# Optimization experiments

Hardware: AMD Instinct MI355X
Metric: run time of the kernel (lower is better)

Reference implementation:

```python
import jax, jax.numpy as jnp
import numpy as np

B, SEQ, D = 2, 1024, 768
E, H = 8, 3072          # num_experts, expert hidden (mlp_ratio=4)
CAPACITY = 2            # k = CAPACITY * num_tokens


def setup_inputs() -> dict:
    key = jax.random.key(0)
    ks = jax.random.split(key, 6)
    x = jax.random.normal(ks[0], (B, SEQ, D), dtype=jnp.float32)
    gate_weight = jax.random.normal(ks[1], (E, D), dtype=jnp.float32) * 0.006
    w1 = jax.random.normal(ks[2], (E, D, H), dtype=jnp.float32) * (1.0 / np.sqrt(D))
    b1 = jnp.zeros((E, H), dtype=jnp.float32)
    w2 = jax.random.normal(ks[3], (E, H, D), dtype=jnp.float32) * (1.0 / np.sqrt(H))
    b2 = jnp.zeros((E, D), dtype=jnp.float32)
    return {"x": x, "gate_weight": gate_weight, "w1": w1, "b1": b1, "w2": w2, "b2": b2}


def reference(x, gate_weight, w1, b1, w2, b2):
    Bb, s, d = x.shape
    xf = x.reshape(-1, d)                     # [S, D]
    S = xf.shape[0]
    k = S * CAPACITY
    logits = xf @ gate_weight.T               # [S, E]
    scores = jax.nn.softmax(logits, axis=-1).T  # [E, S]
    # flattened top-k over all (expert, token) pairs -> sparse gate matrix
    vals, idx = jax.lax.top_k(scores.reshape(-1), k)
    gate = jnp.zeros((E * S,), dtype=x.dtype).at[idx].add(vals).reshape(E, S)
    # expert MLPs (GELU-tanh) applied per expert; zero gate entries kill
    # non-routed (expert, token) pairs -> same math as gather/MLP/scatter.
    h = jax.nn.gelu(jnp.einsum('sd,edh->esh', xf, w1) + b1[:, None, :], approximate=True)
    out = jnp.einsum('esh,ehd->esd', h, w2) + b2[:, None, :]   # [E, S, D]
    y = jnp.einsum('es,esd->sd', gate, out)    # weighted combine + sum over experts
    return y.reshape(Bb, s, d)
```

## Files before the change

kernel.cpp:

```cpp
#include <hip/hip_runtime.h>
#include <math.h>

#define S_TOK 2048
#define NEXP  8
#define DDIM  768
#define HDIM  3072
#define KSEL  4096

typedef __attribute__((ext_vector_type(8))) short short8;
typedef __attribute__((ext_vector_type(4))) float f32x4;
typedef __attribute__((ext_vector_type(2))) unsigned int u32x2;

#define GLOAD_LDS(GP, LP)                                            \
  __builtin_amdgcn_global_load_lds(                                  \
      (__attribute__((address_space(1))) void*)(GP),                 \
      (__attribute__((address_space(3))) void*)(LP), 16, 0, 0)

__device__ __forceinline__ unsigned short f2bf(float f) {
  unsigned u = __float_as_uint(f);
  u += 0x7fffu + ((u >> 16) & 1u);
  return (unsigned short)(u >> 16);
}

__device__ __forceinline__ float gelu_fast(float v) {
  float u = 0.7978845608028654f * (v + 0.044715f * v * v * v);
  float t = __expf(-2.0f * fabsf(u));
  float th = (1.0f - t) / (1.0f + t);
  th = copysignf(th, u);
  return 0.5f * v * (1.0f + th);
}

__global__ __launch_bounds__(256) void zero_kernel(float* __restrict__ p, int n) {
  int i = blockIdx.x * 256 + threadIdx.x;
  if (i < n) p[i] = 0.f;
}

__global__ __launch_bounds__(256) void convx_kernel(const float* __restrict__ x,
                                                    short* __restrict__ xb) {
  int i = (blockIdx.x * 256 + threadIdx.x) * 8;
  float4 a = *(const float4*)(x + i);
  float4 b = *(const float4*)(x + i + 4);
  short8 v;
  v[0] = (short)f2bf(a.x); v[1] = (short)f2bf(a.y);
  v[2] = (short)f2bf(a.z); v[3] = (short)f2bf(a.w);
  v[4] = (short)f2bf(b.x); v[5] = (short)f2bf(b.y);
  v[6] = (short)f2bf(b.z); v[7] = (short)f2bf(b.w);
  *(short8*)(xb + i) = v;
}

__global__ __launch_bounds__(256) void convw_kernel(
    const float* __restrict__ src, short* __restrict__ dst,
    int ncols_src, int col0, int ncols_dst, int row0, int nrows, int nrows_src)
{
  long long i = ((long long)blockIdx.x * 256 + threadIdx.x) * 8;
  int n = (int)(i % ncols_dst);
  long long rr = i / ncols_dst;
  int r = (int)(rr % nrows);
  int e = (int)(rr / nrows);
  const float* s = src + ((size_t)e * nrows_src + row0 + r) * ncols_src + col0 + n;
  float4 a = *(const float4*)(s);
  float4 b = *(const float4*)(s + 4);
  short8 v;
  v[0] = (short)f2bf(a.x); v[1] = (short)f2bf(a.y);
  v[2] = (short)f2bf(a.z); v[3] = (short)f2bf(a.w);
  v[4] = (short)f2bf(b.x); v[5] = (short)f2bf(b.y);
  v[6] = (short)f2bf(b.z); v[7] = (short)f2bf(b.w);
  *(short8*)(dst + i) = v;
}

__global__ __launch_bounds__(256) void gate_kernel(
    const float* __restrict__ x, const float* __restrict__ gw,
    float* __restrict__ scores)
{
  int tid  = threadIdx.x;
  int lane = tid & 63;
  int wid  = tid >> 6;
  int token = blockIdx.x * 4 + wid;
  const float* xr = x + (size_t)token * DDIM;

  float acc[NEXP];
#pragma unroll
  for (int e = 0; e < NEXP; ++e) acc[e] = 0.f;

  for (int d = lane; d < DDIM; d += 64) {
    float xv = xr[d];
#pragma unroll
    for (int e = 0; e < NEXP; ++e) acc[e] += xv * gw[e * DDIM + d];
  }
#pragma unroll
  for (int e = 0; e < NEXP; ++e) {
    for (int off = 32; off; off >>= 1) acc[e] += __shfl_down(acc[e], off, 64);
  }
  if (lane == 0) {
    float m = acc[0];
#pragma unroll
    for (int e = 1; e < NEXP; ++e) m = fmaxf(m, acc[e]);
    float p[NEXP], s = 0.f;
#pragma unroll
    for (int e = 0; e < NEXP; ++e) { p[e] = expf(acc[e] - m); s += p[e]; }
    float inv = 1.0f / s;
#pragma unroll
    for (int e = 0; e < NEXP; ++e) scores[e * S_TOK + token] = p[e] * inv;
  }
}

__device__ unsigned block_scan_excl(unsigned v, volatile unsigned* wsum) {
  int tid = threadIdx.x, lane = tid & 63, wid = tid >> 6;
  __syncthreads();
  unsigned x = v;
#pragma unroll
  for (int off = 1; off < 64; off <<= 1) {
    unsigned t = __shfl_up(x, off, 64);
    if (lane >= off) x += t;
  }
  if (lane == 63) wsum[wid] = x;
  __syncthreads();
  if (tid < 64) {
    unsigned w = (lane < 16) ? wsum[lane] : 0u;
#pragma unroll
    for (int off = 1; off < 16; off <<= 1) {
      unsigned t = __shfl_up(w, off, 64);
      if (lane >= off) w += t;
    }
    if (lane < 16) wsum[lane] = w;
  }
  __syncthreads();
  unsigned woff = (wid > 0) ? wsum[wid - 1] : 0u;
  return woff + (x - v);
}

__global__ __launch_bounds__(1024) void select_kernel(
    const float* __restrict__ scores,
    int* __restrict__ tokenlist, float* __restrict__ slotgate,
    int* __restrict__ offsets)
{
  __shared__ unsigned cnt;
  __shared__ unsigned wsum[16];
  int tid = threadIdx.x;
  int base = tid * 16;

  float sv[16]; unsigned key[16];
#pragma unroll
  for (int j = 0; j < 16; ++j) {
    sv[j] = scores[base + j];
    key[j] = __float_as_uint(sv[j]);
  }

  unsigned lo = 0, hi = 0x3F800000u;
  while (lo < hi) {
    unsigned mid = lo + ((hi - lo + 1) >> 1);
    if (tid == 0) cnt = 0;
    __syncthreads();
    unsigned c = 0;
#pragma unroll
    for (int j = 0; j < 16; ++j) c += (key[j] >= mid) ? 1u : 0u;
    for (int off = 32; off; off >>= 1) c += __shfl_down(c, off, 64);
    if ((tid & 63) == 0) atomicAdd(&cnt, c);
    __syncthreads();
    unsigned tot = cnt;
    __syncthreads();
    if (tot >= (unsigned)KSEL) lo = mid; else hi = mid - 1;
  }
  unsigned V = lo;

  if (tid == 0) cnt = 0;
  __syncthreads();
  {
    unsigned c = 0;
#pragma unroll
    for (int j = 0; j < 16; ++j) c += (key[j] > V) ? 1u : 0u;
    for (int off = 32; off; off >>= 1) c += __shfl_down(c, off, 64);
    if ((tid & 63) == 0) atomicAdd(&cnt, c);
  }
  __syncthreads();
  int need = KSEL - (int)cnt;
  __syncthreads();

  unsigned tloc = 0;
#pragma unroll
  for (int j = 0; j < 16; ++j) tloc += (key[j] == V) ? 1u : 0u;
  unsigned texcl = block_scan_excl(tloc, wsum);

  unsigned selmask = 0, sloc = 0, trun = texcl;
#pragma unroll
  for (int j = 0; j < 16; ++j) {
    bool f;
    if (key[j] > V) f = true;
    else if (key[j] == V) { f = ((int)trun < need); ++trun; }
    else f = false;
    if (f) { selmask |= (1u << j); ++sloc; }
  }
  unsigned sexcl = block_scan_excl(sloc, wsum);

  if ((tid & 127) == 0) offsets[tid >> 7] = (int)sexcl;
  if (tid == 0) offsets[NEXP] = KSEL;

  unsigned p = sexcl;
#pragma unroll
  for (int j = 0; j < 16; ++j) {
    int i = base + j;
    if (selmask & (1u << j)) {
      tokenlist[p] = i & (S_TOK - 1);
      slotgate[p] = sv[j];
      ++p;
    }
  }
}

template <int MODE>
__global__ __launch_bounds__(256) void moe_mfma(
    const short* __restrict__ Abase, const short* __restrict__ Wbf,
    const float* __restrict__ bias, void* __restrict__ outp,
    const int* __restrict__ offsets, const int* __restrict__ tokenlist,
    const float* __restrict__ slotgate,
    int N, int SA, int estride, int split_bits, int cbias, int bias_en)
{
  const int e = (int)blockIdx.x;
  const int tile  = (int)blockIdx.z >> split_bits;
  const int split = (int)blockIdx.z & ((1 << split_bits) - 1);
  const int kb = split * 768;

  const int r0 = offsets[e];
  const int rows = offsets[e + 1] - r0;
  const int rowbase = tile << 7;
  if (rowbase >= rows) return;
  int vr = rows - rowbase; if (vr > 128) vr = 128;
  const int colbase = (int)blockIdx.y << 7;

  __shared__ __align__(16) short As[128 * 32];
  __shared__ __align__(16) short Bs[64 * 64];
  const unsigned bs_lds = (unsigned)(uintptr_t)&Bs[0];

  const int tid = threadIdx.x;
  const int lane = tid & 63;
  const int wid = tid >> 6;
  const int wr = (wid >> 1) << 6;
  const int wc = (wid & 1) << 6;
  const int l15 = lane & 15;
  const int lq = lane >> 4;

  const int row0 = (wid * 2) * 16 + (lane >> 2);
  const int row1 = row0 + 16;
  const int cr0 = (row0 < vr) ? row0 : (vr - 1);
  const int cr1 = (row1 < vr) ? row1 : (vr - 1);
  const short *aptr0, *aptr1;
  if (MODE == 1) {
    aptr0 = Abase + (size_t)tokenlist[r0 + rowbase + cr0] * SA + ((lane & 3) << 3);
    aptr1 = Abase + (size_t)tokenlist[r0 + rowbase + cr1] * SA + ((lane & 3) << 3);
  } else {
    aptr0 = Abase + (size_t)(r0 + rowbase + cr0) * SA + kb + ((lane & 3) << 3);
    aptr1 = Abase + (size_t)(r0 + rowbase + cr1) * SA + kb + ((lane & 3) << 3);
  }

  const short* wb = Wbf + (size_t)e * estride + colbase +
                    ((lane >> 3) << 4) + ((lane & 1) << 3) +
                    (size_t)(kb + ((lane & 7) >> 1)) * N;
  const short* bptr0 = wb + (size_t)(wid * 2 + 0) * 4 * N;
  const short* bptr1 = wb + (size_t)(wid * 2 + 1) * 4 * N;

  const int dst0 = wid * 1024;
  const int dst1 = wid * 1024 + 512;

#define STAGE(K0)                                                 \
  {                                                               \
    GLOAD_LDS(aptr0 + (K0), As + dst0);                           \
    GLOAD_LDS(aptr1 + (K0), As + dst1);                           \
    GLOAD_LDS(bptr0 + (size_t)(K0) * N, Bs + dst0);               \
    GLOAD_LDS(bptr1 + (size_t)(K0) * N, Bs + dst1);               \
  }

  f32x4 acc[4][4];
#pragma unroll
  for (int i = 0; i < 4; ++i)
#pragma unroll
    for (int j = 0; j < 4; ++j) acc[i][j] = (f32x4){0.f, 0.f, 0.f, 0.f};

  STAGE(0);

#pragma unroll 1
  for (int k0 = 0; k0 < 768; k0 += 32) {
    __syncthreads();
    short8 af[4], bfr[4];
#pragma unroll
    for (int i = 0; i < 4; ++i)
      af[i] = *(const short8*)&As[(wr + i * 16 + l15) * 32 + lq * 8];
#pragma unroll
    for (int j = 0; j < 4; ++j) {
      unsigned off = bs_lds + ((unsigned)((lq << 4) + (wc >> 4) + j) << 7) +
                     ((unsigned)l15 << 3);
      union { short8 s; u32x2 u[2]; } fb;
      asm volatile("ds_read_b64_tr_b16 %0, %2 offset:0\n\t"
                   "ds_read_b64_tr_b16 %1, %2 offset:1024"
                   : "=&v"(fb.u[0]), "=&v"(fb.u[1]) : "v"(off));
      bfr[j] = fb.s;
    }
    asm volatile("s_waitcnt lgkmcnt(0)" ::: "memory");
    __builtin_amdgcn_sched_barrier(0);
    __syncthreads();
    if (k0 + 32 < 768) STAGE(k0 + 32);
#pragma unroll
    for (int i = 0; i < 4; ++i)
#pragma unroll
      for (int j = 0; j < 4; ++j)
        acc[i][j] = __builtin_amdgcn_mfma_f32_16x16x32_bf16(af[i], bfr[j], acc[i][j], 0, 0, 0);
  }

  if (MODE == 1) {
    short* hb = (short*)outp;
    const float* bp = bias + (size_t)e * HDIM + cbias + colbase;
#pragma unroll
    for (int i = 0; i < 4; ++i) {
      int rb = wr + i * 16 + lq * 4;
#pragma unroll
      for (int j = 0; j < 4; ++j) {
        int col = wc + j * 16 + l15;
        float bvv = bp[col];
#pragma unroll
        for (int p = 0; p < 4; ++p) {
          int r = rb + p;
          if (r < vr)
            hb[(size_t)(r0 + rowbase + r) * N + colbase + col] =
                (short)f2bf(gelu_fast(acc[i][j][p] + bvv));
        }
      }
    }
  } else {
    float* y = (float*)outp;
    const float* bp = bias + (size_t)e * DDIM + colbase;
    const int addb = (bias_en && split == 0);
#pragma unroll
    for (int i = 0; i < 4; ++i) {
      int rb = wr + i * 16 + lq * 4;
#pragma unroll
      for (int p = 0; p < 4; ++p) {
        int r = rb + p;
        if (r < vr) {
          int gi = r0 + rowbase + r;
          float g = slotgate[gi];
          float* yrow = y + (size_t)tokenlist[gi] * DDIM + colbase;
#pragma unroll
          for (int j = 0; j < 4; ++j) {
            int col = wc + j * 16 + l15;
            float v = acc[i][j][p] + (addb ? bp[col] : 0.f);
            atomicAdd(&yrow[col], g * v);
          }
        }
      }
    }
  }
#undef STAGE
}

extern "C" void kernel_launch(void* const* d_in, const int* in_sizes, int n_in,
                              void* d_out, int out_size, void* d_ws, size_t ws_size,
                              hipStream_t stream) {
  const float* x  = (const float*)d_in[0];
  const float* gw = (const float*)d_in[1];
  const float* w1 = (const float*)d_in[2];
  const float* b1 = (const float*)d_in[3];
  const float* w2 = (const float*)d_in[4];
  const float* b2 = (const float*)d_in[5];
  float* y = (float*)d_out;

  char* ws = (char*)d_ws;
  float* scores    = (float*)(ws);
  int*   tokenlist = (int*)(ws + (64 << 10));
  float* slotgate  = (float*)(ws + (80 << 10));
  int*   offsets   = (int*)(ws + (96 << 10));
  short* xbf       = (short*)(ws + (128 << 10));

  const size_t head = (size_t)(128 << 10) + (size_t)S_TOK * DDIM * 2;
  int nchunk = 2;
  {
    size_t need1 = head + (size_t)NEXP * DDIM * HDIM * 2 + (size_t)KSEL * HDIM * 2;
    if (ws_size >= need1) nchunk = 1;
  }
  const int NC = HDIM / nchunk;
  short* wbf  = (short*)(ws + head);
  short* hbuf = wbf + (size_t)NEXP * DDIM * NC;
  const int estride = DDIM * NC;
  const int sb2 = (NC == 3072) ? 2 : 1;

  zero_kernel<<<(out_size + 255) / 256, 256, 0, stream>>>(y, out_size);
  convx_kernel<<<S_TOK * DDIM / 2048, 256, 0, stream>>>(x, xbf);
  gate_kernel<<<S_TOK / 4, 256, 0, stream>>>(x, gw, scores);
  select_kernel<<<1, 1024, 0, stream>>>(scores, tokenlist, slotgate, offsets);

  for (int c = 0; c < nchunk; ++c) {
    convw_kernel<<<(NEXP * DDIM * NC) / 2048, 256, 0, stream>>>(
        w1, wbf, HDIM, c * NC, NC, 0, DDIM, DDIM);
    dim3 g1(NEXP, NC / 128, 16);
    moe_mfma<1><<<g1, 256, 0, stream>>>(xbf, wbf, b1, hbuf, offsets, tokenlist,
                                        slotgate, NC, DDIM, estride, 0, c * NC, 1);
    convw_kernel<<<(NEXP * NC * DDIM) / 2048, 256, 0, stream>>>(
        w2, wbf, DDIM, 0, DDIM, c * NC, NC, HDIM);
    dim3 g2(NEXP, DDIM / 128, 16 << sb2);
    moe_mfma<2><<<g2, 256, 0, stream>>>(hbuf, wbf, b2, y, offsets, tokenlist,
                                        slotgate, DDIM, NC, estride, sb2, 0, c == 0);
  }
}
```

Baseline: 230.6 us.

## Double-buffer LDS tiles in grouped expert GEMM with explicit vmcnt waits

Splits the A and B shared-memory tiles into two ping-pong buffers and issues global-to-LDS loads two k-steps ahead. Each k-step waits only for the older batch of loads via a partial vmcnt wait before the barrier, so loads overlap with the MFMA work of the previous step. The cost is double the LDS per block, which can lower occupancy, plus hand-managed waitcnt logic that has to stay in step with how many loads are in flight.

```diff
diff --git a/kernel.cpp b/kernel.cpp
--- a/kernel.cpp
+++ b/kernel.cpp
@@ -227,9 +227,12 @@
   int vr = rows - rowbase; if (vr > 128) vr = 128;
   const int colbase = (int)blockIdx.y << 7;
 
-  __shared__ __align__(16) short As[128 * 32];
-  __shared__ __align__(16) short Bs[64 * 64];
-  const unsigned bs_lds = (unsigned)(uintptr_t)&Bs[0];
+  __shared__ __align__(16) short As0[128 * 32];
+  __shared__ __align__(16) short As1[128 * 32];
+  __shared__ __align__(16) short Bs0[64 * 64];
+  __shared__ __align__(16) short Bs1[64 * 64];
+  const unsigned bs0_lds = (unsigned)(uintptr_t)&Bs0[0];
+  const unsigned bs1_lds = (unsigned)(uintptr_t)&Bs1[0];
 
   const int tid = threadIdx.x;
   const int lane = tid & 63;
@@ -261,12 +264,12 @@
   const int dst0 = wid * 1024;
   const int dst1 = wid * 1024 + 512;
 
-#define STAGE(K0)                                                 \
+#define STAGE(K0, ASX, BSX)                                       \
   {                                                               \
-    GLOAD_LDS(aptr0 + (K0), As + dst0);                           \
-    GLOAD_LDS(aptr1 + (K0), As + dst1);                           \
-    GLOAD_LDS(bptr0 + (size_t)(K0) * N, Bs + dst0);               \
-    GLOAD_LDS(bptr1 + (size_t)(K0) * N, Bs + dst1);               \
+    GLOAD_LDS(aptr0 + (K0), (ASX) + dst0);                        \
+    GLOAD_LDS(aptr1 + (K0), (ASX) + dst1);                        \
+    GLOAD_LDS(bptr0 + (size_t)(K0) * N, (BSX) + dst0);            \
+    GLOAD_LDS(bptr1 + (size_t)(K0) * N, (BSX) + dst1);            \
   }
 
   f32x4 acc[4][4];
@@ -275,34 +278,45 @@
 #pragma unroll
     for (int j = 0; j < 4; ++j) acc[i][j] = (f32x4){0.f, 0.f, 0.f, 0.f};
 
-  STAGE(0);
+#define KSTEP_BODY(ASX, BLDS, STG_COND, STG_K, STG_AS, STG_BS, LASTWAIT)   \
+  {                                                               \
+    if (LASTWAIT) { asm volatile("s_waitcnt vmcnt(0)" ::: "memory"); }     \
+    else          { asm volatile("s_waitcnt vmcnt(4)" ::: "memory"); }     \
+    __builtin_amdgcn_s_barrier();                                 \
+    __builtin_amdgcn_sched_barrier(0);                            \
+    short8 af[4], bfr[4];                                         \
+    _Pragma("unroll")                                             \
+    for (int i = 0; i < 4; ++i)                                   \
+      af[i] = *(const short8*)&ASX[(wr + i * 16 + l15) * 32 + lq * 8];     \
+    _Pragma("unroll")                                             \
+    for (int j = 0; j < 4; ++j) {                                 \
+      unsigned off = (BLDS) + ((unsigned)((lq << 4) + (wc >> 4) + j) << 7) + \
+                     ((unsigned)l15 << 3);                        \
+      union { short8 s; u32x2 u[2]; } fb;                         \
+      asm volatile("ds_read_b64_tr_b16 %0, %2 offset:0\n\t"       \
+                   "ds_read_b64_tr_b16 %1, %2 offset:1024"        \
+                   : "=&v"(fb.u[0]), "=&v"(fb.u[1]) : "v"(off));  \
+      bfr[j] = fb.s;                                              \
+    }                                                             \
+    asm volatile("s_waitcnt lgkmcnt(0)" ::: "memory");            \
+    __builtin_amdgcn_sched_barrier(0);                            \
+    __builtin_amdgcn_s_barrier();                                 \
+    __builtin_amdgcn_sched_barrier(0);                            \
+    if (STG_COND) STAGE(STG_K, STG_AS, STG_BS);                   \
+    _Pragma("unroll")                                             \
+    for (int i = 0; i < 4; ++i)                                   \
+      _Pragma("unroll")                                           \
+      for (int j = 0; j < 4; ++j)                                 \
+        acc[i][j] = __builtin_amdgcn_mfma_f32_16x16x32_bf16(af[i], bfr[j], acc[i][j], 0, 0, 0); \
+  }
+
+  STAGE(0, As0, Bs0);
+  STAGE(32, As1, Bs1);
 
 #pragma unroll 1
-  for (int k0 = 0; k0 < 768; k0 += 32) {
-    __syncthreads();
-    short8 af[4], bfr[4];
-#pragma unroll
-    for (int i = 0; i < 4; ++i)
-      af[i] = *(const short8*)&As[(wr + i * 16 + l15) * 32 + lq * 8];
-#pragma unroll
-    for (int j = 0; j < 4; ++j) {
-      unsigned off = bs_lds + ((unsigned)((lq << 4) + (wc >> 4) + j) << 7) +
-                     ((unsigned)l15 << 3);
-      union { short8 s; u32x2 u[2]; } fb;
-      asm volatile("ds_read_b64_tr_b16 %0, %2 offset:0\n\t"
-                   "ds_read_b64_tr_b16 %1, %2 offset:1024"
-                   : "=&v"(fb.u[0]), "=&v"(fb.u[1]) : "v"(off));
-      bfr[j] = fb.s;
-    }
-    asm volatile("s_waitcnt lgkmcnt(0)" ::: "memory");
-    __builtin_amdgcn_sched_barrier(0);
-    __syncthreads();
-    if (k0 + 32 < 768) STAGE(k0 + 32);
-#pragma unroll
-    for (int i = 0; i < 4; ++i)
-#pragma unroll
-      for (int j = 0; j < 4; ++j)
-        acc[i][j] = __builtin_amdgcn_mfma_f32_16x16x32_bf16(af[i], bfr[j], acc[i][j], 0, 0, 0);
+  for (int k0 = 0; k0 < 768; k0 += 64) {
+    KSTEP_BODY(As0, bs0_lds, (k0 + 64 < 768), k0 + 64, As0, Bs0, false);
+    KSTEP_BODY(As1, bs1_lds, (k0 + 96 < 768), k0 + 96, As1, Bs1, (k0 >= 704));
   }
 
   if (MODE == 1) {
@@ -349,6 +363,7 @@
     }
   }
 #undef STAGE
+#undef KSTEP_BODY
 }
 
 extern "C" void kernel_launch(void* const* d_in, const int* in_sizes, int n_in,
```

New measurement: 219.7 us. -4.7%, faster.

## Transpose weights during bf16 conversion, double-buffer GEMM LDS, fuse x conversion into gate

Applied to the files above, without the earlier changes.

The weight-conversion kernel now writes bf16 weights transposed (N-major, K contiguous) through a 32x32 LDS tile, so the GEMM can load B the same way as A and read it with plain 16-byte LDS reads instead of transpose reads. The GEMM main loop becomes double-buffered: the next K-slab is issued before computing the current one, leaving one barrier per iteration. The bf16 conversion of x is folded into the gate kernel, which removes one launch. The trade-off is a transpose kernel that makes scalar 2-byte stores and uses a strided LDS pattern, so it may convert weights more slowly than the old vectorized 8-wide converter. Doubling LDS to 32 KB per block may also lower occupancy.

```diff
diff --git a/kernel.cpp b/kernel.cpp
--- a/kernel.cpp
+++ b/kernel.cpp
@@ -9,7 +9,6 @@
 
 typedef __attribute__((ext_vector_type(8))) short short8;
 typedef __attribute__((ext_vector_type(4))) float f32x4;
-typedef __attribute__((ext_vector_type(2))) unsigned int u32x2;
 
 #define GLOAD_LDS(GP, LP)                                            \
   __builtin_amdgcn_global_load_lds(                                  \
@@ -35,48 +34,39 @@
   if (i < n) p[i] = 0.f;
 }
 
-__global__ __launch_bounds__(256) void convx_kernel(const float* __restrict__ x,
-                                                    short* __restrict__ xb) {
-  int i = (blockIdx.x * 256 + threadIdx.x) * 8;
-  float4 a = *(const float4*)(x + i);
-  float4 b = *(const float4*)(x + i + 4);
-  short8 v;
-  v[0] = (short)f2bf(a.x); v[1] = (short)f2bf(a.y);
-  v[2] = (short)f2bf(a.z); v[3] = (short)f2bf(a.w);
-  v[4] = (short)f2bf(b.x); v[5] = (short)f2bf(b.y);
-  v[6] = (short)f2bf(b.z); v[7] = (short)f2bf(b.w);
-  *(short8*)(xb + i) = v;
-}
-
-__global__ __launch_bounds__(256) void convw_kernel(
+__global__ __launch_bounds__(256) void convwt_kernel(
     const float* __restrict__ src, short* __restrict__ dst,
-    int ncols_src, int col0, int ncols_dst, int row0, int nrows, int nrows_src)
+    int Rsrc, int Csrc, int r0, int c0, int R, int C)
 {
-  long long i = ((long long)blockIdx.x * 256 + threadIdx.x) * 8;
-  int n = (int)(i % ncols_dst);
-  long long rr = i / ncols_dst;
-  int r = (int)(rr % nrows);
-  int e = (int)(rr / nrows);
-  const float* s = src + ((size_t)e * nrows_src + row0 + r) * ncols_src + col0 + n;
-  float4 a = *(const float4*)(s);
-  float4 b = *(const float4*)(s + 4);
-  short8 v;
-  v[0] = (short)f2bf(a.x); v[1] = (short)f2bf(a.y);
-  v[2] = (short)f2bf(a.z); v[3] = (short)f2bf(a.w);
-  v[4] = (short)f2bf(b.x); v[5] = (short)f2bf(b.y);
-  v[6] = (short)f2bf(b.z); v[7] = (short)f2bf(b.w);
-  *(short8*)(dst + i) = v;
+  __shared__ short t[32][33];
+  const int tx = threadIdx.x & 31;
+  const int ty = threadIdx.x >> 5;
+  const int e = (int)blockIdx.z;
+  const int cb = (int)blockIdx.x << 5;
+  const int rb = (int)blockIdx.y << 5;
+#pragma unroll
+  for (int i = 0; i < 4; ++i) {
+    int r = rb + ty + i * 8;
+    t[ty + i * 8][tx] = (short)f2bf(src[((size_t)e * Rsrc + r0 + r) * Csrc + c0 + cb + tx]);
+  }
+  __syncthreads();
+#pragma unroll
+  for (int i = 0; i < 4; ++i) {
+    int cg = cb + ty + i * 8;
+    dst[((size_t)e * C + cg) * R + rb + tx] = t[tx][ty + i * 8];
+  }
 }
 
 __global__ __launch_bounds__(256) void gate_kernel(
     const float* __restrict__ x, const float* __restrict__ gw,
-    float* __restrict__ scores)
+    float* __restrict__ scores, short* __restrict__ xb)
 {
   int tid  = threadIdx.x;
   int lane = tid & 63;
   int wid  = tid >> 6;
   int token = blockIdx.x * 4 + wid;
   const float* xr = x + (size_t)token * DDIM;
+  short* xbr = xb + (size_t)token * DDIM;
 
   float acc[NEXP];
 #pragma unroll
@@ -84,6 +74,7 @@
 
   for (int d = lane; d < DDIM; d += 64) {
     float xv = xr[d];
+    xbr[d] = (short)f2bf(xv);
 #pragma unroll
     for (int e = 0; e < NEXP; ++e) acc[e] += xv * gw[e * DDIM + d];
   }
@@ -209,11 +200,11 @@
 
 template <int MODE>
 __global__ __launch_bounds__(256) void moe_mfma(
-    const short* __restrict__ Abase, const short* __restrict__ Wbf,
+    const short* __restrict__ Abase, const short* __restrict__ Wt,
     const float* __restrict__ bias, void* __restrict__ outp,
     const int* __restrict__ offsets, const int* __restrict__ tokenlist,
     const float* __restrict__ slotgate,
-    int N, int SA, int estride, int split_bits, int cbias, int bias_en)
+    int N, int SA, int WROW, long long estride, int split_bits, int cbias, int bias_en)
 {
   const int e = (int)blockIdx.x;
   const int tile  = (int)blockIdx.z >> split_bits;
@@ -227,9 +218,8 @@
   int vr = rows - rowbase; if (vr > 128) vr = 128;
   const int colbase = (int)blockIdx.y << 7;
 
-  __shared__ __align__(16) short As[128 * 32];
-  __shared__ __align__(16) short Bs[64 * 64];
-  const unsigned bs_lds = (unsigned)(uintptr_t)&Bs[0];
+  __shared__ __align__(16) short As[2][128 * 32];
+  __shared__ __align__(16) short Bs[2][128 * 32];
 
   const int tid = threadIdx.x;
   const int lane = tid & 63;
@@ -251,22 +241,19 @@
     aptr0 = Abase + (size_t)(r0 + rowbase + cr0) * SA + kb + ((lane & 3) << 3);
     aptr1 = Abase + (size_t)(r0 + rowbase + cr1) * SA + kb + ((lane & 3) << 3);
   }
-
-  const short* wb = Wbf + (size_t)e * estride + colbase +
-                    ((lane >> 3) << 4) + ((lane & 1) << 3) +
-                    (size_t)(kb + ((lane & 7) >> 1)) * N;
-  const short* bptr0 = wb + (size_t)(wid * 2 + 0) * 4 * N;
-  const short* bptr1 = wb + (size_t)(wid * 2 + 1) * 4 * N;
+  const short* wtb = Wt + (size_t)e * estride + ((lane & 3) << 3) + kb;
+  const short* bptr0 = wtb + (size_t)(colbase + row0) * WROW;
+  const short* bptr1 = wtb + (size_t)(colbase + row1) * WROW;
 
   const int dst0 = wid * 1024;
   const int dst1 = wid * 1024 + 512;
 
-#define STAGE(K0)                                                 \
+#define STAGE(K0, BUF)                                            \
   {                                                               \
-    GLOAD_LDS(aptr0 + (K0), As + dst0);                           \
-    GLOAD_LDS(aptr1 + (K0), As + dst1);                           \
-    GLOAD_LDS(bptr0 + (size_t)(K0) * N, Bs + dst0);               \
-    GLOAD_LDS(bptr1 + (size_t)(K0) * N, Bs + dst1);               \
+    GLOAD_LDS(aptr0 + (K0), &As[BUF][dst0]);                      \
+    GLOAD_LDS(aptr1 + (K0), &As[BUF][dst1]);                      \
+    GLOAD_LDS(bptr0 + (K0), &Bs[BUF][dst0]);                      \
+    GLOAD_LDS(bptr1 + (K0), &Bs[BUF][dst1]);                      \
   }
 
   f32x4 acc[4][4];
@@ -275,34 +262,29 @@
 #pragma unroll
     for (int j = 0; j < 4; ++j) acc[i][j] = (f32x4){0.f, 0.f, 0.f, 0.f};
 
-  STAGE(0);
-
+  STAGE(0, 0);
+  __syncthreads();
+
+  int cur = 0;
 #pragma unroll 1
   for (int k0 = 0; k0 < 768; k0 += 32) {
+    if (k0 + 32 < 768) STAGE(k0 + 32, cur ^ 1);
+    const short* Asl = As[cur];
+    const short* Bsl = Bs[cur];
+    short8 af[4], bf[4];
+#pragma unroll
+    for (int i = 0; i < 4; ++i)
+      af[i] = *(const short8*)&Asl[(wr + i * 16 + l15) * 32 + lq * 8];
+#pragma unroll
+    for (int j = 0; j < 4; ++j)
+      bf[j] = *(const short8*)&Bsl[(wc + j * 16 + l15) * 32 + lq * 8];
+#pragma unroll
+    for (int i = 0; i < 4; ++i)
+#pragma unroll
+      for (int j = 0; j < 4; ++j)
+        acc[i][j] = __builtin_amdgcn_mfma_f32_16x16x32_bf16(af[i], bf[j], acc[i][j], 0, 0, 0);
     __syncthreads();
-    short8 af[4], bfr[4];
-#pragma unroll
-    for (int i = 0; i < 4; ++i)
-      af[i] = *(const short8*)&As[(wr + i * 16 + l15) * 32 + lq * 8];
-#pragma unroll
-    for (int j = 0; j < 4; ++j) {
-      unsigned off = bs_lds + ((unsigned)((lq << 4) + (wc >> 4) + j) << 7) +
-                     ((unsigned)l15 << 3);
-      union { short8 s; u32x2 u[2]; } fb;
-      asm volatile("ds_read_b64_tr_b16 %0, %2 offset:0\n\t"
-                   "ds_read_b64_tr_b16 %1, %2 offset:1024"
-                   : "=&v"(fb.u[0]), "=&v"(fb.u[1]) : "v"(off));
-      bfr[j] = fb.s;
-    }
-    asm volatile("s_waitcnt lgkmcnt(0)" ::: "memory");
-    __builtin_amdgcn_sched_barrier(0);
-    __syncthreads();
-    if (k0 + 32 < 768) STAGE(k0 + 32);
-#pragma unroll
-    for (int i = 0; i < 4; ++i)
-#pragma unroll
-      for (int j = 0; j < 4; ++j)
-        acc[i][j] = __builtin_amdgcn_mfma_f32_16x16x32_bf16(af[i], bfr[j], acc[i][j], 0, 0, 0);
+    cur ^= 1;
   }
 
   if (MODE == 1) {
@@ -378,24 +360,27 @@
   const int NC = HDIM / nchunk;
   short* wbf  = (short*)(ws + head);
   short* hbuf = wbf + (size_t)NEXP * DDIM * NC;
-  const int estride = DDIM * NC;
+  const long long estride = (long long)DDIM * NC;
   const int sb2 = (NC == 3072) ? 2 : 1;
 
   zero_kernel<<<(out_size + 255) / 256, 256, 0, stream>>>(y, out_size);
-  convx_kernel<<<S_TOK * DDIM / 2048, 256, 0, stream>>>(x, xbf);
-  gate_kernel<<<S_TOK / 4, 256, 0, stream>>>(x, gw, scores);
+  gate_kernel<<<S_TOK / 4, 256, 0, stream>>>(x, gw, scores, xbf);
   select_kernel<<<1, 1024, 0, stream>>>(scores, tokenlist, slotgate, offsets);
 
   for (int c = 0; c < nchunk; ++c) {
-    convw_kernel<<<(NEXP * DDIM * NC) / 2048, 256, 0, stream>>>(
-        w1, wbf, HDIM, c * NC, NC, 0, DDIM, DDIM);
+    {
+      dim3 gt(NC / 32, DDIM / 32, NEXP);
+      convwt_kernel<<<gt, 256, 0, stream>>>(w1, wbf, DDIM, HDIM, 0, c * NC, DDIM, NC);
+    }
     dim3 g1(NEXP, NC / 128, 16);
     moe_mfma<1><<<g1, 256, 0, stream>>>(xbf, wbf, b1, hbuf, offsets, tokenlist,
-                                        slotgate, NC, DDIM, estride, 0, c * NC, 1);
-    convw_kernel<<<(NEXP * NC * DDIM) / 2048, 256, 0, stream>>>(
-        w2, wbf, DDIM, 0, DDIM, c * NC, NC, HDIM);
+                                        slotgate, NC, DDIM, DDIM, estride, 0, c * NC, 1);
+    {
+      dim3 gt(DDIM / 32, NC / 32, NEXP);
+      convwt_kernel<<<gt, 256, 0, stream>>>(w2, wbf, HDIM, DDIM, c * NC, 0, NC, DDIM);
+    }
     dim3 g2(NEXP, DDIM / 128, 16 << sb2);
     moe_mfma<2><<<g2, 256, 0, stream>>>(hbuf, wbf, b2, y, offsets, tokenlist,
-                                        slotgate, DDIM, NC, estride, sb2, 0, c == 0);
-  }
-}
+                                        slotgate, DDIM, NC, NC, estride, sb2, 0, c == 0);
+  }
+}
```

Result: no change. 232.6 us (+0.9%).
